# Optimization experiments

Hardware: AMD Instinct MI355X
Metric: run time of the kernel (lower is better)

## Reference

```python
import jax, jax.numpy as jnp
from jax import lax
import numpy as np

P = 9          # patch_size (hardcoded in CUTSEncoder)
HALF = P // 2  # 4
EPS = 1e-5     # BatchNorm eps (torch default)
SLOPE = 0.01   # LeakyReLU negative slope (torch default)


def _conv(x, w, b):
    # 3x3 'same' conv, NCHW / OIHW
    y = lax.conv_general_dilated(x, w, (1, 1), 'SAME',
                                 dimension_numbers=('NCHW', 'OIHW', 'NCHW'))
    return y + b[None, :, None, None]


def _bn(x, gamma, beta):
    # training-mode BatchNorm2d: batch statistics over (N,H,W)
    m = jnp.mean(x, axis=(0, 2, 3), keepdims=True)
    v = jnp.var(x, axis=(0, 2, 3), keepdims=True)
    return gamma[None, :, None, None] * (x - m) * lax.rsqrt(v + EPS) + beta[None, :, None, None]


def _block(x, w, b, g, be):
    return jax.nn.leaky_relu(_bn(_conv(x, w, b), g, be), SLOPE)


def setup_inputs() -> dict:
    key = jax.random.key(0)
    ks = jax.random.split(key, 16)
    B, C, H, W = 8, 3, 256, 256
    K = 32                 # num_kernels
    L = K * 8              # latent_dim = 256
    S = 32                 # sampled_patches_per_image

    x = jax.random.normal(ks[0], (B, C, H, W), jnp.float32)
    anchors_hw = jax.random.randint(ks[1], (B, S, 2), HALF, H - HALF, jnp.int32)
    positives_hw = jax.random.randint(ks[2], (B, S, 2), HALF, H - HALF, jnp.int32)

    def w_(k, shape):
        return jax.random.normal(k, shape, jnp.float32) * 0.05

    params = {
        'w1': w_(ks[3], (K, C, 3, 3)),       'b1': jnp.zeros((K,), jnp.float32),
        'g1': jnp.ones((K,), jnp.float32),   'be1': jnp.zeros((K,), jnp.float32),
        'w2': w_(ks[4], (2 * K, K, 3, 3)),   'b2': jnp.zeros((2 * K,), jnp.float32),
        'g2': jnp.ones((2 * K,), jnp.float32), 'be2': jnp.zeros((2 * K,), jnp.float32),
        'w3': w_(ks[5], (4 * K, 2 * K, 3, 3)), 'b3': jnp.zeros((4 * K,), jnp.float32),
        'g3': jnp.ones((4 * K,), jnp.float32), 'be3': jnp.zeros((4 * K,), jnp.float32),
        'w4': w_(ks[6], (8 * K, 4 * K, 3, 3)), 'b4': jnp.zeros((8 * K,), jnp.float32),
        'g4': jnp.ones((8 * K,), jnp.float32), 'be4': jnp.zeros((8 * K,), jnp.float32),
        'rw': w_(ks[7], (S * C * P * P, S * L)),  # recon Linear [out,in]
        'rb': jnp.zeros((S * C * P * P,), jnp.float32),
    }
    return dict(x=x, anchors_hw=anchors_hw, positives_hw=positives_hw, **params)


def reference(x, anchors_hw, positives_hw,
              w1, b1, g1, be1, w2, b2, g2, be2,
              w3, b3, g3, be3, w4, b4, g4, be4, rw, rb):
    B, C, H, W = x.shape
    # 4-stage conv+BN+LeakyReLU backbone -> z: [B, L, H, W]
    z = _block(x, w1, b1, g1, be1)
    z = _block(z, w2, b2, g2, be2)
    z = _block(z, w3, b3, g3, be3)
    z = _block(z, w4, b4, g4, be4)

    # batched 9x9 patch extraction around anchors: [B, S, C, P, P]
    def patch(img, hw):  # img: [C,H,W], hw: [2]
        return lax.dynamic_slice(img, (0, hw[0] - HALF, hw[1] - HALF), (C, P, P))
    x_anchors = jax.vmap(lambda img, hws: jax.vmap(lambda hw: patch(img, hw))(hws))(x, anchors_hw)

    # batched pointwise latent gathers: [B, S, L]
    def gather_z(zb, hws):  # zb: [L,H,W]
        return zb[:, hws[:, 0], hws[:, 1]].T  # [S, L]
    z_anchors = jax.vmap(gather_z)(z, anchors_hw)
    z_positives = jax.vmap(gather_z)(z, positives_hw)

    x_anchors_flat = x_anchors.reshape(B, -1)
    x_recon = z_anchors.reshape(B, -1) @ rw.T + rb
    return (z, x_anchors_flat, x_recon, z_anchors, z_positives)
```

## Files before the change

### kernel.cpp

```cpp
#include <hip/hip_runtime.h>
#include <hip/hip_bf16.h>

#define HW 65536
constexpr int IMG_W = 256;

typedef __attribute__((ext_vector_type(8))) short short8;
typedef __attribute__((ext_vector_type(4))) float f32x4;

__device__ __forceinline__ float bf2f(unsigned short u) {
    return __uint_as_float(((unsigned)u) << 16);
}
__device__ __forceinline__ unsigned short f2bf(float f) {
    __hip_bfloat16 h = __float2bfloat16(f);
    return *reinterpret_cast<unsigned short*>(&h);
}

__global__ __launch_bounds__(256) void conv1_direct(
    const float* __restrict__ x, const float* __restrict__ wt,
    const float* __restrict__ bias, unsigned short* __restrict__ outraw)
{
    constexpr int CIN = 3, COUT = 32, OCB = 16;
    const int tile = blockIdx.x;
    const int ty0 = (tile >> 3) << 5;
    const int tx0 = (tile & 7) << 5;
    const int oc0 = blockIdx.y * OCB;
    const int b = blockIdx.z;

    __shared__ alignas(16) float s_in[CIN][34][36];
    __shared__ alignas(16) float s_w[CIN][9][OCB];

    const int tid = threadIdx.x;
    const int lx = tid & 31;
    const int ly = tid >> 5;

    float acc[4][OCB];
    #pragma unroll
    for (int j = 0; j < 4; ++j)
        #pragma unroll
        for (int oc = 0; oc < OCB; ++oc) acc[j][oc] = 0.f;

    for (int idx = tid; idx < CIN * 34 * 34; idx += 256) {
        int ic  = idx / (34 * 34);
        int rem = idx - ic * (34 * 34);
        int r   = rem / 34;
        int cc  = rem - r * 34;
        int gy = ty0 - 1 + r, gx = tx0 - 1 + cc;
        float v = 0.f;
        if ((unsigned)gy < 256u && (unsigned)gx < 256u)
            v = x[((size_t)(b * CIN + ic)) * HW + (size_t)gy * IMG_W + gx];
        s_in[ic][r][cc] = v;
    }
    for (int idx = tid; idx < CIN * 9 * OCB; idx += 256) {
        int oc  = idx & (OCB - 1);
        int t2  = idx >> 4;
        int tap = t2 % 9;
        int ic  = t2 / 9;
        s_w[ic][tap][oc] = wt[((size_t)(oc0 + oc) * CIN + ic) * 9 + tap];
    }
    __syncthreads();

    for (int ic = 0; ic < CIN; ++ic) {
        #pragma unroll
        for (int tap = 0; tap < 9; ++tap) {
            const int dy = tap / 3, dx = tap % 3;
            float wr[OCB];
            #pragma unroll
            for (int q = 0; q < OCB / 4; ++q)
                *(float4*)&wr[q * 4] = *(const float4*)&s_w[ic][tap][q * 4];
            #pragma unroll
            for (int j = 0; j < 4; ++j) {
                float iv = s_in[ic][ly + 8 * j + dy][lx + dx];
                #pragma unroll
                for (int oc = 0; oc < OCB; ++oc) acc[j][oc] += iv * wr[oc];
            }
        }
    }

    #pragma unroll
    for (int j = 0; j < 4; ++j) {
        const size_t p = ((size_t)b << 16) + (size_t)((ty0 + ly + 8 * j) << 8) + tx0 + lx;
        short8 v0, v1;
        #pragma unroll
        for (int k = 0; k < 8; ++k) {
            v0[k] = (short)f2bf(acc[j][k] + bias[oc0 + k]);
            v1[k] = (short)f2bf(acc[j][8 + k] + bias[oc0 + 8 + k]);
        }
        *(short8*)&outraw[p * COUT + oc0]     = v0;
        *(short8*)&outraw[p * COUT + oc0 + 8] = v1;
    }
}

__global__ void repack2(const float* __restrict__ w, unsigned short* __restrict__ wp,
                        int COUT, int CIN)
{
    int i = blockIdx.x * 256 + threadIdx.x;
    int K9 = 9 * CIN;
    if (i >= COUT * K9) return;
    int oc = i / K9, k = i - oc * K9;
    int tap = k / CIN, ic = k - tap * CIN;
    wp[(size_t)(k >> 3) * COUT * 8 + oc * 8 + (k & 7)] =
        f2bf(w[((size_t)(oc * CIN + ic)) * 9 + tap]);
}

template<int CIN, int COUT, int WM, int WN, int WOC, int MINW>
__global__ __launch_bounds__(256, MINW) void conv_mfma5(
    const unsigned short* __restrict__ in, const float2* __restrict__ coef,
    const unsigned short* __restrict__ wp, const float* __restrict__ bias,
    unsigned short* __restrict__ outraw, float2* __restrict__ partial)
{
    static_assert(WM * WN == 4 && WN * WOC == COUT, "bad wave geometry");
    constexpr int CINP = CIN + 8;
    constexpr int ROWS = WM * 4;
    constexpr int NOCT = CIN / 8;
    constexpr int NG = WOC / 16;
    constexpr int ICB = CIN / 32;
    constexpr int TILES = 65536 / (ROWS * 16);
    constexpr int NCH = (ROWS + 2) * 18 * NOCT;
    constexpr int CPT = (NCH + 255) / 256;

    __shared__ alignas(16) short s_in[(ROWS + 2) * 18 * CINP];
    __shared__ float2 s_coef[CIN];

    const int tile = blockIdx.x;
    const int b = blockIdx.z;
    const int ty0 = (tile >> 4) * ROWS;
    const int tx0 = (tile & 15) * 16;
    const int tid = threadIdx.x;

    if (tid < CIN) s_coef[tid] = coef[tid];

    const size_t bbase = (size_t)b << 16;
    short8 stg[CPT];
    #pragma unroll
    for (int i = 0; i < CPT; ++i) {
        const int idx = tid + i * 256;
        const int ic8 = idx & (NOCT - 1);
        const int rc  = idx / NOCT;
        const int c = rc % 18, r = rc / 18;
        const int gy = ty0 - 1 + r, gx = tx0 - 1 + c;
        stg[i] = (short8)0;
        if (idx < NCH && (unsigned)gy < 256u && (unsigned)gx < 256u)
            stg[i] = *(const short8*)&in[(bbase + (size_t)(gy << 8) + gx) * CIN + ic8 * 8];
    }
    __syncthreads();

    #pragma unroll
    for (int i = 0; i < CPT; ++i) {
        const int idx = tid + i * 256;
        if (idx < NCH) {
            const int ic8 = idx & (NOCT - 1);
            const int rc  = idx / NOCT;
            const int c = rc % 18, r = rc / 18;
            const int gy = ty0 - 1 + r, gx = tx0 - 1 + c;
            short8 v = (short8)0;
            if ((unsigned)gy < 256u && (unsigned)gx < 256u) {
                #pragma unroll
                for (int j = 0; j < 8; ++j) {
                    float2 ab = s_coef[ic8 * 8 + j];
                    float xv = fmaf(ab.x, bf2f((unsigned short)stg[i][j]), ab.y);
                    xv = fmaxf(xv, 0.01f * xv);
                    v[j] = (short)f2bf(xv);
                }
            }
            *(short8*)&s_in[(r * 18 + c) * CINP + ic8 * 8] = v;
        }
    }
    __syncthreads();

    const int lane = tid & 63;
    const int wv = tid >> 6;
    const int wm = wv / WN, wn = wv % WN;
    const int ln = lane & 15;
    const int grp = lane >> 4;

    f32x4 acc[4][NG] = {};

    const unsigned short* wpb = wp + ((size_t)grp * COUT + wn * WOC + ln) * 8;

    for (int tap = 0; tap < 9; ++tap) {
        const int dy = tap / 3, dx = tap - dy * 3;
        const int arow = (wm * 4 + dy) * 18 + ln + dx;
        const int kc0 = tap * (CIN / 8);
        #pragma unroll
        for (int icb = 0; icb < ICB; ++icb) {
            short8 wfr[NG];
            #pragma unroll
            for (int g = 0; g < NG; ++g)
                wfr[g] = *(const short8*)&wpb[((size_t)(kc0 + icb * 4) * COUT + g * 16) * 8];
            #pragma unroll
            for (int f = 0; f < 4; ++f) {
                short8 px = *(const short8*)&s_in[(arow + f * 18) * CINP + icb * 32 + grp * 8];
                #pragma unroll
                for (int g = 0; g < NG; ++g)
                    acc[f][g] = __builtin_amdgcn_mfma_f32_16x16x32_bf16(wfr[g], px, acc[f][g], 0, 0, 0);
            }
        }
    }

    const size_t pchunk = ((size_t)(b * TILES + tile) * WM + wm) * COUT;
    #pragma unroll
    for (int g = 0; g < NG; ++g) {
        const int ocl = wn * WOC + g * 16 + grp * 4;
        const f32x4 b4 = *(const f32x4*)&bias[ocl];
        f32x4 vs = {}, vq = {};
        #pragma unroll
        for (int f = 0; f < 4; ++f) {
            const int row = ty0 + wm * 4 + f;
            f32x4 v = acc[f][g] + b4;
            vs += v; vq += v * v;
            short4 sv;
            sv.x = (short)f2bf(v[0]); sv.y = (short)f2bf(v[1]);
            sv.z = (short)f2bf(v[2]); sv.w = (short)f2bf(v[3]);
            *(short4*)&outraw[(bbase + (size_t)(row << 8) + tx0 + ln) * COUT + ocl] = sv;
        }
        #pragma unroll
        for (int d = 1; d < 16; d <<= 1) {
            #pragma unroll
            for (int r = 0; r < 4; ++r) {
                vs[r] += __shfl_xor(vs[r], d);
                vq[r] += __shfl_xor(vq[r], d);
            }
        }
        if (ln == 0) {
            #pragma unroll
            for (int r = 0; r < 4; ++r)
                partial[pchunk + ocl + r] = make_float2(vs[r], vq[r]);
        }
    }
}

template<int C>
__global__ __launch_bounds__(256) void bn_stats_nhwc(const unsigned short* __restrict__ raw,
                                                     float2* __restrict__ partial)
{
    constexpr int CPT = C / 8;
    constexpr int PPI = 256 / CPT;
    const int t = threadIdx.x;
    const int co = t % CPT, pg = t / CPT;
    const int p0 = blockIdx.x * 2048;
    float s[8], ss[8];
    #pragma unroll
    for (int j = 0; j < 8; ++j) { s[j] = 0.f; ss[j] = 0.f; }
    for (int p = p0 + pg; p < p0 + 2048; p += PPI) {
        short8 v = *(const short8*)&raw[(size_t)p * C + co * 8];
        #pragma unroll
        for (int j = 0; j < 8; ++j) {
            float xv = bf2f((unsigned short)v[j]);
            s[j] += xv; ss[j] += xv * xv;
        }
    }
    __shared__ float rs[256][8], rss[256][8];
    #pragma unroll
    for (int j = 0; j < 8; ++j) { rs[t][j] = s[j]; rss[t][j] = ss[j]; }
    __syncthreads();
    for (int off = PPI / 2; off > 0; off >>= 1) {
        if (pg < off) {
            #pragma unroll
            for (int j = 0; j < 8; ++j) {
                rs[t][j]  += rs[t + off * CPT][j];
                rss[t][j] += rss[t + off * CPT][j];
            }
        }
        __syncthreads();
    }
    if (pg == 0) {
        #pragma unroll
        for (int j = 0; j < 8; ++j)
            partial[(size_t)(co * 8 + j) * 256 + blockIdx.x] = make_float2(rs[t][j], rss[t][j]);
    }
}

__global__ void bn_finalize_kernel(const float2* __restrict__ partial,
                                   const float* __restrict__ gamma,
                                   const float* __restrict__ beta,
                                   float2* __restrict__ coef, int C, int nchunk)
{
    int c = threadIdx.x;
    if (c >= C) return;
    float s = 0.f, ss = 0.f;
    for (int i = 0; i < nchunk; ++i) {
        float2 p = partial[(size_t)c * nchunk + i];
        s += p.x; ss += p.y;
    }
    const float N = 524288.f;
    float m = s / N;
    float v = ss / N - m * m;
    float rsq = rsqrtf(v + 1e-5f);
    float a = gamma[c] * rsq;
    coef[c] = make_float2(a, beta[c] - m * a);
}

template<int C, int NCHUNK>
__global__ __launch_bounds__(256) void bn_finalize3(const float2* __restrict__ partial,
                                                    const float* __restrict__ gamma,
                                                    const float* __restrict__ beta,
                                                    float2* __restrict__ coef)
{
    const int c = blockIdx.x, t = threadIdx.x;
    float s = 0.f, q = 0.f;
    for (int i = t; i < NCHUNK; i += 256) {
        float2 p = partial[(size_t)i * C + c];
        s += p.x; q += p.y;
    }
    __shared__ float rs[256], rq[256];
    rs[t] = s; rq[t] = q;
    __syncthreads();
    for (int off = 128; off; off >>= 1) {
        if (t < off) { rs[t] += rs[t + off]; rq[t] += rq[t + off]; }
        __syncthreads();
    }
    if (t == 0) {
        const float N = 524288.f;
        float m = rs[0] / N;
        float v = rq[0] / N - m * m;
        float a = gamma[c] * rsqrtf(v + 1e-5f);
        coef[c] = make_float2(a, beta[c] - m * a);
    }
}

__global__ __launch_bounds__(256) void apply_t(const unsigned short* __restrict__ raw,
                                               const float2* __restrict__ coef,
                                               float* __restrict__ z)
{
    __shared__ float s_t[256 * 36];
    __shared__ float2 s_c[256];
    const int t = threadIdx.x;
    s_c[t] = coef[t];
    __syncthreads();

    const size_t p0 = (size_t)blockIdx.x * 32;
    const int o = t & 31, prow = t >> 5;
    #pragma unroll
    for (int it = 0; it < 4; ++it) {
        const int pxi = prow + it * 8;
        short8 v = *(const short8*)&raw[(p0 + pxi) * 256 + o * 8];
        #pragma unroll
        for (int j = 0; j < 8; ++j) {
            const int oc = o * 8 + j;
            float2 ab = s_c[oc];
            float xv = fmaf(ab.x, bf2f((unsigned short)v[j]), ab.y);
            xv = fmaxf(xv, 0.01f * xv);
            s_t[oc * 36 + (pxi ^ ((o & 7) * 4))] = xv;
        }
    }
    __syncthreads();

    const int Q = t & 7, ocr = t >> 3;
    const int b = (int)(p0 >> 16);
    const int pxl = (int)(p0 & 65535);
    #pragma unroll
    for (int pass = 0; pass < 8; ++pass) {
        const int oc = ocr + pass * 32;
        const int w = (oc >> 3) & 7;
        f32x4 vv = *(const f32x4*)&s_t[oc * 36 + ((Q ^ w) * 4)];
        *(f32x4*)&z[(((size_t)(b * 256 + oc)) << 16) + pxl + Q * 4] = vv;
    }
}

__global__ void patches_kernel(const float* __restrict__ x, const int* __restrict__ hw,
                               float* __restrict__ out)
{
    int bs = blockIdx.x;
    int b = bs >> 5;
    int h = hw[bs * 2], w = hw[bs * 2 + 1];
    int t = threadIdx.x;
    if (t < 243) {
        int c = t / 81, r = (t / 9) % 9, cc = t % 9;
        out[(size_t)bs * 243 + t] =
            x[((size_t)(b * 3 + c)) * HW + (size_t)(h - 4 + r) * IMG_W + (w - 4 + cc)];
    }
}

__global__ void gather_kernel(const float* __restrict__ z, const int* __restrict__ hw,
                              float* __restrict__ out)
{
    int bs = blockIdx.x;
    int b = bs >> 5;
    int h = hw[bs * 2], w = hw[bs * 2 + 1];
    int l = threadIdx.x;
    out[(size_t)bs * 256 + l] = z[((size_t)(b * 256 + l)) * HW + (size_t)h * IMG_W + w];
}

__global__ __launch_bounds__(256) void recon_kernel(const float* __restrict__ za,
                                                    const float* __restrict__ rw,
                                                    const float* __restrict__ rb,
                                                    float* __restrict__ out)
{
    int wave = threadIdx.x >> 6, lane = threadIdx.x & 63;
    int n0 = blockIdx.x * 16 + wave * 4;
    float acc[4][8];
    #pragma unroll
    for (int j = 0; j < 4; ++j)
        #pragma unroll
        for (int bb = 0; bb < 8; ++bb) acc[j][bb] = 0.f;

    for (int i = 0; i < 32; ++i) {
        int k = i * 256 + lane * 4;
        float4 wv[4];
        #pragma unroll
        for (int j = 0; j < 4; ++j)
            wv[j] = *(const float4*)&rw[(size_t)(n0 + j) * 8192 + k];
        #pragma unroll
        for (int bb = 0; bb < 8; ++bb) {
            float4 zv = *(const float4*)&za[(size_t)bb * 8192 + k];
            #pragma unroll
            for (int j = 0; j < 4; ++j)
                acc[j][bb] += zv.x * wv[j].x + zv.y * wv[j].y + zv.z * wv[j].z + zv.w * wv[j].w;
        }
    }
    #pragma unroll
    for (int j = 0; j < 4; ++j)
        #pragma unroll
        for (int bb = 0; bb < 8; ++bb) {
            float v = acc[j][bb];
            #pragma unroll
            for (int off = 32; off; off >>= 1) v += __shfl_down(v, off);
            if (lane == 0) out[(size_t)bb * 7776 + n0 + j] = v + rb[n0 + j];
        }
}

extern "C" void kernel_launch(void* const* d_in, const int* in_sizes, int n_in,
                              void* d_out, int out_size, void* d_ws, size_t ws_size,
                              hipStream_t stream) {
    (void)in_sizes; (void)n_in; (void)out_size; (void)ws_size;

    const float* x        = (const float*)d_in[0];
    const int* anchors    = (const int*)d_in[1];
    const int* positives  = (const int*)d_in[2];
    const float* w1 = (const float*)d_in[3];  const float* b1 = (const float*)d_in[4];
    const float* g1 = (const float*)d_in[5];  const float* be1 = (const float*)d_in[6];
    const float* w2 = (const float*)d_in[7];  const float* b2 = (const float*)d_in[8];
    const float* g2 = (const float*)d_in[9];  const float* be2 = (const float*)d_in[10];
    const float* w3 = (const float*)d_in[11]; const float* b3 = (const float*)d_in[12];
    const float* g3 = (const float*)d_in[13]; const float* be3 = (const float*)d_in[14];
    const float* w4 = (const float*)d_in[15]; const float* b4 = (const float*)d_in[16];
    const float* g4 = (const float*)d_in[17]; const float* be4 = (const float*)d_in[18];
    const float* rw = (const float*)d_in[19]; const float* rb = (const float*)d_in[20];

    float* z  = (float*)d_out;
    float* xa = z + 134217728;
    float* xr = xa + 62208;
    float* za = xr + 62208;
    float* zp = za + 65536;

    char* zb = (char*)d_out;
    unsigned short* raw1 = (unsigned short*)zb;
    unsigned short* raw2 = (unsigned short*)(zb + 33554432ull);
    unsigned short* raw3 = (unsigned short*)(zb + 100663296ull);

    char* ws = (char*)d_ws;
    unsigned short* wp   = (unsigned short*)ws;
    float2* partial = (float2*)(ws + 1048576ull);
    float2* coef1   = (float2*)(ws + 17825792ull);
    float2* coef2   = coef1 + 256;
    float2* coef3   = coef2 + 256;
    float2* coef4   = coef3 + 256;
    unsigned short* raw4 = (unsigned short*)(ws + 18874368ull);

    conv1_direct<<<dim3(64, 2, 8), 256, 0, stream>>>(x, w1, b1, raw1);
    bn_stats_nhwc<32><<<256, 256, 0, stream>>>(raw1, partial);
    bn_finalize_kernel<<<1, 256, 0, stream>>>(partial, g1, be1, coef1, 32, 256);

    repack2<<<(64 * 288 + 255) / 256, 256, 0, stream>>>(w2, wp, 64, 32);
    conv_mfma5<32, 64, 4, 1, 64, 3><<<dim3(256, 1, 8), 256, 0, stream>>>(raw1, coef1, wp, b2, raw2, partial);
    bn_finalize3<64, 8192><<<64, 256, 0, stream>>>(partial, g2, be2, coef2);

    repack2<<<(128 * 576 + 255) / 256, 256, 0, stream>>>(w3, wp, 128, 64);
    conv_mfma5<64, 128, 2, 2, 64, 3><<<dim3(512, 1, 8), 256, 0, stream>>>(raw2, coef2, wp, b3, raw3, partial);
    bn_finalize3<128, 8192><<<128, 256, 0, stream>>>(partial, g3, be3, coef3);

    repack2<<<(256 * 1152 + 255) / 256, 256, 0, stream>>>(w4, wp, 256, 128);
    conv_mfma5<128, 256, 2, 2, 128, 2><<<dim3(512, 1, 8), 256, 0, stream>>>(raw3, coef3, wp, b4, raw4, partial);
    bn_finalize3<256, 8192><<<256, 256, 0, stream>>>(partial, g4, be4, coef4);

    apply_t<<<16384, 256, 0, stream>>>(raw4, coef4, z);

    patches_kernel<<<256, 256, 0, stream>>>(x, anchors, xa);
    gather_kernel<<<256, 256, 0, stream>>>(z, anchors, za);
    gather_kernel<<<256, 256, 0, stream>>>(z, positives, zp);
    recon_kernel<<<486, 256, 0, stream>>>(za, rw, rb, xr);
}
```

Measured before the change: 866.0 us.

## Reorder conv MFMA loops to reuse LDS row fragments across vertical taps

Restructures the implicit-GEMM conv inner loop so that, for each input-channel block and horizontal offset, six row fragments are loaded once from shared memory and reused across the three vertical taps and four output rows. Before, each of those fragments was reloaded for every tap. It also fixes the wave output-channel width at 64 and changes conv4 to a 1x4 wave geometry with twice as many, shorter tiles. This lets occupancy hints stay at 3 waves per SIMD, at the cost of more halo reloading per tile.

```diff
diff --git a/kernel.cpp b/kernel.cpp
--- a/kernel.cpp
+++ b/kernel.cpp
@@ -102,17 +102,18 @@
         f2bf(w[((size_t)(oc * CIN + ic)) * 9 + tap]);
 }
 
-template<int CIN, int COUT, int WM, int WN, int WOC, int MINW>
-__global__ __launch_bounds__(256, MINW) void conv_mfma5(
+template<int CIN, int COUT, int WM, int WN>
+__global__ __launch_bounds__(256, 3) void conv_mfma7(
     const unsigned short* __restrict__ in, const float2* __restrict__ coef,
     const unsigned short* __restrict__ wp, const float* __restrict__ bias,
     unsigned short* __restrict__ outraw, float2* __restrict__ partial)
 {
+    constexpr int WOC = 64;
+    constexpr int NG = 4;
     static_assert(WM * WN == 4 && WN * WOC == COUT, "bad wave geometry");
     constexpr int CINP = CIN + 8;
     constexpr int ROWS = WM * 4;
     constexpr int NOCT = CIN / 8;
-    constexpr int NG = WOC / 16;
     constexpr int ICB = CIN / 32;
     constexpr int TILES = 65536 / (ROWS * 16);
     constexpr int NCH = (ROWS + 2) * 18 * NOCT;
@@ -176,23 +177,29 @@
     f32x4 acc[4][NG] = {};
 
     const unsigned short* wpb = wp + ((size_t)grp * COUT + wn * WOC + ln) * 8;
-
-    for (int tap = 0; tap < 9; ++tap) {
-        const int dy = tap / 3, dx = tap - dy * 3;
-        const int arow = (wm * 4 + dy) * 18 + ln + dx;
-        const int kc0 = tap * (CIN / 8);
-        #pragma unroll
-        for (int icb = 0; icb < ICB; ++icb) {
-            short8 wfr[NG];
-            #pragma unroll
-            for (int g = 0; g < NG; ++g)
-                wfr[g] = *(const short8*)&wpb[((size_t)(kc0 + icb * 4) * COUT + g * 16) * 8];
-            #pragma unroll
-            for (int f = 0; f < 4; ++f) {
-                short8 px = *(const short8*)&s_in[(arow + f * 18) * CINP + icb * 32 + grp * 8];
+    const int fb = (wm * 4) * 18 + ln;
+
+    for (int icb = 0; icb < ICB; ++icb) {
+        const int ko = icb * 32 + grp * 8;
+        for (int dx = 0; dx < 3; ++dx) {
+            short8 frag[6];
+            #pragma unroll
+            for (int r = 0; r < 6; ++r)
+                frag[r] = *(const short8*)&s_in[(fb + r * 18 + dx) * CINP + ko];
+            #pragma unroll
+            for (int dy = 0; dy < 3; ++dy) {
+                const int kc0 = (dy * 3 + dx) * (CIN / 8) + icb * 4;
+                short8 wfr[NG];
                 #pragma unroll
                 for (int g = 0; g < NG; ++g)
-                    acc[f][g] = __builtin_amdgcn_mfma_f32_16x16x32_bf16(wfr[g], px, acc[f][g], 0, 0, 0);
+                    wfr[g] = *(const short8*)&wpb[((size_t)kc0 * COUT + g * 16) * 8];
+                #pragma unroll
+                for (int f = 0; f < 4; ++f) {
+                    #pragma unroll
+                    for (int g = 0; g < NG; ++g)
+                        acc[f][g] = __builtin_amdgcn_mfma_f32_16x16x32_bf16(
+                            wfr[g], frag[dy + f], acc[f][g], 0, 0, 0);
+                }
             }
         }
     }
@@ -462,15 +469,15 @@
     bn_finalize_kernel<<<1, 256, 0, stream>>>(partial, g1, be1, coef1, 32, 256);
 
     repack2<<<(64 * 288 + 255) / 256, 256, 0, stream>>>(w2, wp, 64, 32);
-    conv_mfma5<32, 64, 4, 1, 64, 3><<<dim3(256, 1, 8), 256, 0, stream>>>(raw1, coef1, wp, b2, raw2, partial);
+    conv_mfma7<32, 64, 4, 1><<<dim3(256, 1, 8), 256, 0, stream>>>(raw1, coef1, wp, b2, raw2, partial);
     bn_finalize3<64, 8192><<<64, 256, 0, stream>>>(partial, g2, be2, coef2);
 
     repack2<<<(128 * 576 + 255) / 256, 256, 0, stream>>>(w3, wp, 128, 64);
-    conv_mfma5<64, 128, 2, 2, 64, 3><<<dim3(512, 1, 8), 256, 0, stream>>>(raw2, coef2, wp, b3, raw3, partial);
+    conv_mfma7<64, 128, 2, 2><<<dim3(512, 1, 8), 256, 0, stream>>>(raw2, coef2, wp, b3, raw3, partial);
     bn_finalize3<128, 8192><<<128, 256, 0, stream>>>(partial, g3, be3, coef3);
 
     repack2<<<(256 * 1152 + 255) / 256, 256, 0, stream>>>(w4, wp, 256, 128);
-    conv_mfma5<128, 256, 2, 2, 128, 2><<<dim3(512, 1, 8), 256, 0, stream>>>(raw3, coef3, wp, b4, raw4, partial);
+    conv_mfma7<128, 256, 1, 4><<<dim3(1024, 1, 8), 256, 0, stream>>>(raw3, coef3, wp, b4, raw4, partial);
     bn_finalize3<256, 8192><<<256, 256, 0, stream>>>(partial, g4, be4, coef4);
 
     apply_t<<<16384, 256, 0, stream>>>(raw4, coef4, z);
```

After: 835.1 us. -3.6%, faster.
